# Kernel optimization log

Measured on AMD Instinct MI355X. Metric: run time of the kernel, lower is better.

## Reference

```python
import jax, jax.numpy as jnp
import numpy as np

N = 50000      # nodes
E = 800000     # edges
XS = 64        # x_size
ES = 32        # edge_attr dim (in_size = XS + ES = 96)
OUT = 64       # out_size
H = 128        # hidden_size
EPS = 1e-5


def _lin_init(k, fan_in, fan_out):
    s = 1.0 / np.sqrt(fan_in)
    kw, kb = jax.random.split(k)
    w = jax.random.uniform(kw, (fan_in, fan_out), minval=-s, maxval=s, dtype=jnp.float32)
    b = jax.random.uniform(kb, (fan_out,), minval=-s, maxval=s, dtype=jnp.float32)
    return w, b


def setup_inputs() -> dict:
    key = jax.random.key(0)
    ks = jax.random.split(key, 12)
    x = jax.random.normal(ks[0], (N, XS), dtype=jnp.float32)
    edge_index = jax.random.randint(ks[1], (2, E), 0, N, dtype=jnp.int64)
    edge_attr = jax.random.normal(ks[2], (E, ES), dtype=jnp.float32)
    u = jax.random.normal(ks[3], (1, 8), dtype=jnp.float32)
    batch = jnp.zeros((N,), dtype=jnp.int64)
    # MLP1: (96->128) LReLU (128->128) LReLU (128->64) LReLU LN(64)
    m1w0, m1b0 = _lin_init(ks[4], XS + ES, H)
    m1w1, m1b1 = _lin_init(ks[5], H, H)
    m1w2, m1b2 = _lin_init(ks[6], H, OUT)
    ln1_g = jnp.ones((OUT,), jnp.float32); ln1_b = jnp.zeros((OUT,), jnp.float32)
    # MLP2: (128->128) LReLU (128->128) LReLU (128->64) LReLU LN(64)
    m2w0, m2b0 = _lin_init(ks[7], XS + OUT, H)
    m2w1, m2b1 = _lin_init(ks[8], H, H)
    m2w2, m2b2 = _lin_init(ks[9], H, OUT)
    ln2_g = jnp.ones((OUT,), jnp.float32); ln2_b = jnp.zeros((OUT,), jnp.float32)
    return dict(x=x, edge_index=edge_index, edge_attr=edge_attr, u=u, batch=batch,
                m1w0=m1w0, m1b0=m1b0, m1w1=m1w1, m1b1=m1b1, m1w2=m1w2, m1b2=m1b2,
                ln1_g=ln1_g, ln1_b=ln1_b,
                m2w0=m2w0, m2b0=m2b0, m2w1=m2w1, m2b1=m2b1, m2w2=m2w2, m2b2=m2b2,
                ln2_g=ln2_g, ln2_b=ln2_b)


def _lrelu(v):
    return jax.nn.leaky_relu(v, 0.01)


def _layernorm(v, g, b):
    mu = jnp.mean(v, axis=-1, keepdims=True)
    var = jnp.mean(jnp.square(v - mu), axis=-1, keepdims=True)
    return (v - mu) * jax.lax.rsqrt(var + EPS) * g + b


def _mlp(h, w0, b0, w1, b1, w2, b2, g, bn):
    h = _lrelu(h @ w0 + b0)
    h = _lrelu(h @ w1 + b1)
    h = _lrelu(h @ w2 + b2)          # activate_last=True
    return _layernorm(h, g, bn)      # layer_norm=True


def reference(x, edge_index, edge_attr, u, batch,
              m1w0, m1b0, m1w1, m1b1, m1w2, m1b2, ln1_g, ln1_b,
              m2w0, m2b0, m2w1, m2b1, m2w2, m2b2, ln2_g, ln2_b):
    row, col = edge_index[0], edge_index[1]
    # gather source nodes, concat edge features -> per-edge MLP
    h = jnp.concatenate([x[row], edge_attr], axis=1)            # [E, 96]
    h = _mlp(h, m1w0, m1b0, m1w1, m1b1, m1w2, m1b2, ln1_g, ln1_b)  # [E, 64]
    # scatter_mean over destination nodes
    agg = jax.ops.segment_sum(h, col, num_segments=N)           # [N, 64]
    cnt = jax.ops.segment_sum(jnp.ones((E,), h.dtype), col, num_segments=N)
    agg = agg / jnp.maximum(cnt, 1.0)[:, None]
    # node update MLP
    h2 = jnp.concatenate([x, agg], axis=1)                      # [N, 128]
    return _mlp(h2, m2w0, m2b0, m2w1, m2b1, m2w2, m2b2, ln2_g, ln2_b)
```

## Files before the change

### kernel.cpp

```cpp
#include <hip/hip_runtime.h>


#define NNODES 50000
#define NEDGES 800000
#define NTILES_E 6250
#define NTILES_N 391

typedef __bf16 bf16;
typedef __bf16 __attribute__((ext_vector_type(4))) bf16x4;
typedef __bf16 __attribute__((ext_vector_type(8))) bf16x8;
typedef float __attribute__((ext_vector_type(4))) f32x4;

__device__ __forceinline__ f32x4 mfma_bf16(bf16x8 a, bf16x8 b, f32x4 c) {
    return __builtin_amdgcn_mfma_f32_16x16x32_bf16(a, b, c, 0, 0, 0);
}

__global__ void prep_weights(const float* __restrict__ w10, const float* __restrict__ w11,
                             const float* __restrict__ w12, const float* __restrict__ w20,
                             const float* __restrict__ w21, const float* __restrict__ w22,
                             bf16* __restrict__ img) {
    int idx = blockIdx.x * 256 + threadIdx.x;
    float f;
    if (idx < 13312) {
        int n = idx / 104, k = idx % 104;
        f = (k < 96) ? w10[k * 128 + n] : 0.0f;
    } else if (idx < 30720) {
        int t = idx - 13312; int n = t / 136, k = t % 136;
        f = (k < 128) ? w11[k * 128 + n] : 0.0f;
    } else if (idx < 39424) {
        int t = idx - 30720; int n = t / 136, k = t % 136;
        f = (k < 128) ? w12[k * 64 + n] : 0.0f;
    } else if (idx < 56832) {
        int t = idx - 39424; int n = t / 136, k = t % 136;
        f = (k < 128) ? w20[k * 128 + n] : 0.0f;
    } else if (idx < 74240) {
        int t = idx - 56832; int n = t / 136, k = t % 136;
        f = (k < 128) ? w21[k * 128 + n] : 0.0f;
    } else if (idx < 82944) {
        int t = idx - 74240; int n = t / 136, k = t % 136;
        f = (k < 128) ? w22[k * 64 + n] : 0.0f;
    } else {
        return;
    }
    img[idx] = (bf16)f;
}

__global__ void hist_kernel(const int* __restrict__ col, int* __restrict__ hist) {
    int i = blockIdx.x * 512 + threadIdx.x;
    if (i < NEDGES) {
        int d = col[i];
        if ((unsigned)d < (unsigned)NNODES) atomicAdd(hist + d, 1);
    }
}

__global__ void scanA(const int* __restrict__ hist, int* __restrict__ off,
                      int* __restrict__ csum) {
    __shared__ int sd[512];
    int t = threadIdx.x, i = blockIdx.x * 512 + t;
    int v = (i < NNODES) ? hist[i] : 0;
    sd[t] = v;
    __syncthreads();
    for (int o2 = 1; o2 < 512; o2 <<= 1) {
        int x = (t >= o2) ? sd[t - o2] : 0;
        __syncthreads();
        sd[t] += x;
        __syncthreads();
    }
    if (i < NNODES) off[i] = sd[t] - v;
    if (t == 511) csum[blockIdx.x] = sd[511];
}

__global__ void scanB(int* __restrict__ csum) {
    __shared__ int sd[128];
    int t = threadIdx.x;
    int v = (t < 98) ? csum[t] : 0;
    sd[t] = v;
    __syncthreads();
    for (int o2 = 1; o2 < 128; o2 <<= 1) {
        int x = (t >= o2) ? sd[t - o2] : 0;
        __syncthreads();
        sd[t] += x;
        __syncthreads();
    }
    if (t < 98) csum[t] = sd[t] - v;
}

__global__ void scanC(int* __restrict__ off, const int* __restrict__ csum) {
    int i = blockIdx.x * 512 + threadIdx.x;
    if (i < NNODES) off[i] += csum[blockIdx.x];
}

__global__ void scatter_kernel(const int* __restrict__ eidx, int* __restrict__ off,
                               int* __restrict__ perm, int* __restrict__ rdS) {
    int i = blockIdx.x * 512 + threadIdx.x;
    if (i < NEDGES) {
        int r = eidx[i], d = eidx[NEDGES + i];
        if ((unsigned)d < (unsigned)NNODES && (unsigned)r < (unsigned)NNODES) {
            int pos = atomicAdd(off + d, 1);
            if ((unsigned)pos < (unsigned)NEDGES) {
                perm[pos] = i;
                rdS[pos] = (int)(((unsigned)r & 0xFFFFu) | ((unsigned)d << 16));
            }
        }
    }
}

__global__ __launch_bounds__(256) void edge_mlp(
    const float* __restrict__ x, const int* __restrict__ perm,
    const int* __restrict__ rdS, const float* __restrict__ eattr,
    const bf16* __restrict__ wimg,
    const float* __restrict__ b0g, const float* __restrict__ b1g,
    const float* __restrict__ b2g, const float* __restrict__ lng,
    const float* __restrict__ lnb, float* __restrict__ agg) {
    __shared__ __align__(16) bf16 wall[39424];
    __shared__ __align__(16) bf16 atile[128 * 104];
    __shared__ __align__(16) bf16 hid[128 * 136];
    __shared__ float bs[448];
    __shared__ int dstile[128];

    const int tid = threadIdx.x;
    {
        const uint4* src = (const uint4*)wimg;
        uint4* dst = (uint4*)wall;
        for (int i = tid; i < 4928; i += 256) dst[i] = src[i];
    }
    if (tid < 128) { bs[tid] = b0g[tid]; bs[128 + tid] = b1g[tid]; }
    else {
        int t = tid - 128;
        if (t < 64) { bs[256 + t] = b2g[t]; bs[320 + t] = lng[t]; bs[384 + t] = lnb[t]; }
    }
    __syncthreads();

    const int lane = tid & 63;
    const int wv = tid >> 6;
    const int col16 = lane & 15;
    const int quad = lane >> 4;

    float b0r[8], b1r[8], b2r[4], gr[4], br[4];
#pragma unroll
    for (int i = 0; i < 8; i++) { b0r[i] = bs[i * 16 + col16]; b1r[i] = bs[128 + i * 16 + col16]; }
#pragma unroll
    for (int i = 0; i < 4; i++) {
        b2r[i] = bs[256 + i * 16 + col16];
        gr[i] = bs[320 + i * 16 + col16];
        br[i] = bs[384 + i * 16 + col16];
    }

    const bf16* w0t = wall;
    const bf16* w1t = wall + 13312;
    const bf16* w2t = wall + 30720;

    const f32x4 vzero = {0.0f, 0.0f, 0.0f, 0.0f};
    const int r0 = wv * 32 + col16;
    const int rw = wv * 32 + quad * 4;
    const int el = tid >> 1, half = tid & 1;

    for (int tile = blockIdx.x; tile < NTILES_E; tile += gridDim.x) {
        const int sbase = tile * 128;
        {
            const int s = sbase + el;
            const unsigned v = (unsigned)rdS[s];
            int e = perm[s];
            int r = (int)(v & 0xFFFFu);
            unsigned d = v >> 16;
            if (r >= NNODES) r = 0;
            if ((unsigned)e >= (unsigned)NEDGES) e = 0;
            if (half == 0) dstile[el] = (d < (unsigned)NNODES) ? (int)d : 0;
            const float4* xs = (const float4*)(x + (size_t)r * 64);
            bf16* arow = atile + el * 104;
#pragma unroll
            for (int j = 0; j < 8; j++) {
                float4 vv = xs[half * 8 + j];
                bf16x4 u = {(bf16)vv.x, (bf16)vv.y, (bf16)vv.z, (bf16)vv.w};
                *(bf16x4*)(arow + half * 32 + j * 4) = u;
            }
            const float4* es = (const float4*)(eattr + (size_t)e * 32);
#pragma unroll
            for (int j = 0; j < 4; j++) {
                float4 vv = es[half * 4 + j];
                bf16x4 u = {(bf16)vv.x, (bf16)vv.y, (bf16)vv.z, (bf16)vv.w};
                *(bf16x4*)(arow + 64 + half * 16 + j * 4) = u;
            }
        }
        __syncthreads();

        f32x4 acc1[2][8];
#pragma unroll
        for (int mt = 0; mt < 2; mt++)
#pragma unroll
            for (int nt = 0; nt < 8; nt++) acc1[mt][nt] = vzero;
#pragma unroll
        for (int ks = 0; ks < 3; ks++) {
            bf16x8 a0 = *(const bf16x8*)(atile + r0 * 104 + ks * 32 + quad * 8);
            bf16x8 a1 = *(const bf16x8*)(atile + (r0 + 16) * 104 + ks * 32 + quad * 8);
#pragma unroll
            for (int nt = 0; nt < 8; nt++) {
                bf16x8 b = *(const bf16x8*)(w0t + (nt * 16 + col16) * 104 + ks * 32 + quad * 8);
                acc1[0][nt] = mfma_bf16(a0, b, acc1[0][nt]);
                acc1[1][nt] = mfma_bf16(a1, b, acc1[1][nt]);
            }
        }
#pragma unroll
        for (int mt = 0; mt < 2; mt++)
#pragma unroll
            for (int nt = 0; nt < 8; nt++)
#pragma unroll
                for (int rg = 0; rg < 4; rg++) {
                    float v = acc1[mt][nt][rg] + b0r[nt];
                    v = (v > 0.0f) ? v : 0.01f * v;
                    hid[(rw + mt * 16 + rg) * 136 + nt * 16 + col16] = (bf16)v;
                }

        bf16x8 a2[2][4];
#pragma unroll
        for (int mt = 0; mt < 2; mt++)
#pragma unroll
            for (int ks = 0; ks < 4; ks++)
                a2[mt][ks] = *(const bf16x8*)(hid + (r0 + mt * 16) * 136 + ks * 32 + quad * 8);
        f32x4 acc2[2][8];
#pragma unroll
        for (int mt = 0; mt < 2; mt++)
#pragma unroll
            for (int nt = 0; nt < 8; nt++) acc2[mt][nt] = vzero;
#pragma unroll
        for (int ks = 0; ks < 4; ks++) {
#pragma unroll
            for (int nt = 0; nt < 8; nt++) {
                bf16x8 b = *(const bf16x8*)(w1t + (nt * 16 + col16) * 136 + ks * 32 + quad * 8);
                acc2[0][nt] = mfma_bf16(a2[0][ks], b, acc2[0][nt]);
                acc2[1][nt] = mfma_bf16(a2[1][ks], b, acc2[1][nt]);
            }
        }
#pragma unroll
        for (int mt = 0; mt < 2; mt++)
#pragma unroll
            for (int nt = 0; nt < 8; nt++)
#pragma unroll
                for (int rg = 0; rg < 4; rg++) {
                    float v = acc2[mt][nt][rg] + b1r[nt];
                    v = (v > 0.0f) ? v : 0.01f * v;
                    hid[(rw + mt * 16 + rg) * 136 + nt * 16 + col16] = (bf16)v;
                }

        bf16x8 a3[2][4];
#pragma unroll
        for (int mt = 0; mt < 2; mt++)
#pragma unroll
            for (int ks = 0; ks < 4; ks++)
                a3[mt][ks] = *(const bf16x8*)(hid + (r0 + mt * 16) * 136 + ks * 32 + quad * 8);
        f32x4 acc3[2][4];
#pragma unroll
        for (int mt = 0; mt < 2; mt++)
#pragma unroll
            for (int nt = 0; nt < 4; nt++) acc3[mt][nt] = vzero;
#pragma unroll
        for (int ks = 0; ks < 4; ks++) {
#pragma unroll
            for (int nt = 0; nt < 4; nt++) {
                bf16x8 b = *(const bf16x8*)(w2t + (nt * 16 + col16) * 136 + ks * 32 + quad * 8);
                acc3[0][nt] = mfma_bf16(a3[0][ks], b, acc3[0][nt]);
                acc3[1][nt] = mfma_bf16(a3[1][ks], b, acc3[1][nt]);
            }
        }

#pragma unroll
        for (int mt = 0; mt < 2; mt++) {
            float vals[4][4];
            float s1[4] = {0.f, 0.f, 0.f, 0.f}, s2[4] = {0.f, 0.f, 0.f, 0.f};
#pragma unroll
            for (int nt = 0; nt < 4; nt++)
#pragma unroll
                for (int rg = 0; rg < 4; rg++) {
                    float v = acc3[mt][nt][rg] + b2r[nt];
                    v = (v > 0.0f) ? v : 0.01f * v;
                    vals[nt][rg] = v;
                    s1[rg] += v;
                    s2[rg] += v * v;
                }
#pragma unroll
            for (int off2 = 1; off2 < 16; off2 <<= 1) {
#pragma unroll
                for (int rg = 0; rg < 4; rg++) {
                    s1[rg] += __shfl_xor(s1[rg], off2);
                    s2[rg] += __shfl_xor(s2[rg], off2);
                }
            }
            float o[4][4];
            int dr[4];
#pragma unroll
            for (int rg = 0; rg < 4; rg++) {
                float mu = s1[rg] * 0.015625f;
                float var = s2[rg] * 0.015625f - mu * mu;
                float rstd = rsqrtf(var + 1e-5f);
                int c = dstile[rw + mt * 16 + rg];
                dr[rg] = ((unsigned)c < (unsigned)NNODES) ? c : 0;
#pragma unroll
                for (int nt = 0; nt < 4; nt++)
                    o[nt][rg] = (vals[nt][rg] - mu) * rstd * gr[nt] + br[nt];
            }
            float run0 = o[0][0], run1 = o[1][0], run2 = o[2][0], run3 = o[3][0];
            int cur = dr[0];
#pragma unroll
            for (int rg = 1; rg < 4; rg++) {
                if (dr[rg] != cur) {
                    float* dst = agg + (size_t)cur * 64 + col16;
                    atomicAdd(dst, run0); atomicAdd(dst + 16, run1);
                    atomicAdd(dst + 32, run2); atomicAdd(dst + 48, run3);
                    run0 = o[0][rg]; run1 = o[1][rg]; run2 = o[2][rg]; run3 = o[3][rg];
                    cur = dr[rg];
                } else {
                    run0 += o[0][rg]; run1 += o[1][rg]; run2 += o[2][rg]; run3 += o[3][rg];
                }
            }
            float* dst = agg + (size_t)cur * 64 + col16;
            atomicAdd(dst, run0); atomicAdd(dst + 16, run1);
            atomicAdd(dst + 32, run2); atomicAdd(dst + 48, run3);
        }
        __syncthreads();
    }
}

__global__ __launch_bounds__(256) void node_mlp(
    const float* __restrict__ x, const float* __restrict__ agg,
    const int* __restrict__ hist, const bf16* __restrict__ wimg,
    const float* __restrict__ b0g, const float* __restrict__ b1g,
    const float* __restrict__ b2g, const float* __restrict__ lng,
    const float* __restrict__ lnb, float* __restrict__ out) {
    __shared__ __align__(16) bf16 wall[43520];
    __shared__ __align__(16) bf16 atile[128 * 136];
    __shared__ __align__(16) bf16 hid[128 * 136];
    __shared__ float bs[448];

    const int tid = threadIdx.x;
    {
        const uint4* src = (const uint4*)wimg;
        uint4* dst = (uint4*)wall;
        for (int i = tid; i < 5440; i += 256) dst[i] = src[i];
    }
    if (tid < 128) { bs[tid] = b0g[tid]; bs[128 + tid] = b1g[tid]; }
    else {
        int t = tid - 128;
        if (t < 64) { bs[256 + t] = b2g[t]; bs[320 + t] = lng[t]; bs[384 + t] = lnb[t]; }
    }
    __syncthreads();

    const int lane = tid & 63;
    const int wv = tid >> 6;
    const int col16 = lane & 15;
    const int quad = lane >> 4;

    float b0r[8], b1r[8], b2r[4], gr[4], br[4];
#pragma unroll
    for (int i = 0; i < 8; i++) { b0r[i] = bs[i * 16 + col16]; b1r[i] = bs[128 + i * 16 + col16]; }
#pragma unroll
    for (int i = 0; i < 4; i++) {
        b2r[i] = bs[256 + i * 16 + col16];
        gr[i] = bs[320 + i * 16 + col16];
        br[i] = bs[384 + i * 16 + col16];
    }

    const bf16* w0t = wall;
    const bf16* w1t = wall + 17408;
    const bf16* w2t = wall + 34816;

    const f32x4 vzero = {0.0f, 0.0f, 0.0f, 0.0f};
    const int r0 = wv * 32 + col16;
    const int rw = wv * 32 + quad * 4;
    const int el = tid >> 1, half = tid & 1;

    for (int tile = blockIdx.x; tile < NTILES_N; tile += gridDim.x) {
        const int nbase = tile * 128;
        {
            int i = nbase + el;
            if (i >= NNODES) i = NNODES - 1;
            const float4* xs = (const float4*)(x + (size_t)i * 64);
            bf16* arow = atile + el * 136;
#pragma unroll
            for (int j = 0; j < 8; j++) {
                float4 v = xs[half * 8 + j];
                bf16x4 u = {(bf16)v.x, (bf16)v.y, (bf16)v.z, (bf16)v.w};
                *(bf16x4*)(arow + half * 32 + j * 4) = u;
            }
            int c = hist[i];
            float inv = 1.0f / (float)(c > 1 ? c : 1);
            const float4* as = (const float4*)(agg + (size_t)i * 64);
#pragma unroll
            for (int j = 0; j < 8; j++) {
                float4 v = as[half * 8 + j];
                bf16x4 u = {(bf16)(v.x * inv), (bf16)(v.y * inv), (bf16)(v.z * inv), (bf16)(v.w * inv)};
                *(bf16x4*)(arow + 64 + half * 32 + j * 4) = u;
            }
        }
        __syncthreads();

        f32x4 acc1[2][8];
#pragma unroll
        for (int mt = 0; mt < 2; mt++)
#pragma unroll
            for (int nt = 0; nt < 8; nt++) acc1[mt][nt] = vzero;
#pragma unroll
        for (int ks = 0; ks < 4; ks++) {
            bf16x8 a0 = *(const bf16x8*)(atile + r0 * 136 + ks * 32 + quad * 8);
            bf16x8 a1 = *(const bf16x8*)(atile + (r0 + 16) * 136 + ks * 32 + quad * 8);
#pragma unroll
            for (int nt = 0; nt < 8; nt++) {
                bf16x8 b = *(const bf16x8*)(w0t + (nt * 16 + col16) * 136 + ks * 32 + quad * 8);
                acc1[0][nt] = mfma_bf16(a0, b, acc1[0][nt]);
                acc1[1][nt] = mfma_bf16(a1, b, acc1[1][nt]);
            }
        }
#pragma unroll
        for (int mt = 0; mt < 2; mt++)
#pragma unroll
            for (int nt = 0; nt < 8; nt++)
#pragma unroll
                for (int rg = 0; rg < 4; rg++) {
                    float v = acc1[mt][nt][rg] + b0r[nt];
                    v = (v > 0.0f) ? v : 0.01f * v;
                    hid[(rw + mt * 16 + rg) * 136 + nt * 16 + col16] = (bf16)v;
                }

        bf16x8 a2[2][4];
#pragma unroll
        for (int mt = 0; mt < 2; mt++)
#pragma unroll
            for (int ks = 0; ks < 4; ks++)
                a2[mt][ks] = *(const bf16x8*)(hid + (r0 + mt * 16) * 136 + ks * 32 + quad * 8);
        f32x4 acc2[2][8];
#pragma unroll
        for (int mt = 0; mt < 2; mt++)
#pragma unroll
            for (int nt = 0; nt < 8; nt++) acc2[mt][nt] = vzero;
#pragma unroll
        for (int ks = 0; ks < 4; ks++) {
#pragma unroll
            for (int nt = 0; nt < 8; nt++) {
                bf16x8 b = *(const bf16x8*)(w1t + (nt * 16 + col16) * 136 + ks * 32 + quad * 8);
                acc2[0][nt] = mfma_bf16(a2[0][ks], b, acc2[0][nt]);
                acc2[1][nt] = mfma_bf16(a2[1][ks], b, acc2[1][nt]);
            }
        }
#pragma unroll
        for (int mt = 0; mt < 2; mt++)
#pragma unroll
            for (int nt = 0; nt < 8; nt++)
#pragma unroll
                for (int rg = 0; rg < 4; rg++) {
                    float v = acc2[mt][nt][rg] + b1r[nt];
                    v = (v > 0.0f) ? v : 0.01f * v;
                    hid[(rw + mt * 16 + rg) * 136 + nt * 16 + col16] = (bf16)v;
                }

        bf16x8 a3[2][4];
#pragma unroll
        for (int mt = 0; mt < 2; mt++)
#pragma unroll
            for (int ks = 0; ks < 4; ks++)
                a3[mt][ks] = *(const bf16x8*)(hid + (r0 + mt * 16) * 136 + ks * 32 + quad * 8);
        f32x4 acc3[2][4];
#pragma unroll
        for (int mt = 0; mt < 2; mt++)
#pragma unroll
            for (int nt = 0; nt < 4; nt++) acc3[mt][nt] = vzero;
#pragma unroll
        for (int ks = 0; ks < 4; ks++) {
#pragma unroll
            for (int nt = 0; nt < 4; nt++) {
                bf16x8 b = *(const bf16x8*)(w2t + (nt * 16 + col16) * 136 + ks * 32 + quad * 8);
                acc3[0][nt] = mfma_bf16(a3[0][ks], b, acc3[0][nt]);
                acc3[1][nt] = mfma_bf16(a3[1][ks], b, acc3[1][nt]);
            }
        }

#pragma unroll
        for (int mt = 0; mt < 2; mt++) {
            float vals[4][4];
            float s1[4] = {0.f, 0.f, 0.f, 0.f}, s2[4] = {0.f, 0.f, 0.f, 0.f};
#pragma unroll
            for (int nt = 0; nt < 4; nt++)
#pragma unroll
                for (int rg = 0; rg < 4; rg++) {
                    float v = acc3[mt][nt][rg] + b2r[nt];
                    v = (v > 0.0f) ? v : 0.01f * v;
                    vals[nt][rg] = v;
                    s1[rg] += v;
                    s2[rg] += v * v;
                }
#pragma unroll
            for (int off2 = 1; off2 < 16; off2 <<= 1) {
#pragma unroll
                for (int rg = 0; rg < 4; rg++) {
                    s1[rg] += __shfl_xor(s1[rg], off2);
                    s2[rg] += __shfl_xor(s2[rg], off2);
                }
            }
#pragma unroll
            for (int rg = 0; rg < 4; rg++) {
                float mu = s1[rg] * 0.015625f;
                float var = s2[rg] * 0.015625f - mu * mu;
                float rstd = rsqrtf(var + 1e-5f);
                int i = nbase + rw + mt * 16 + rg;
                if (i < NNODES) {
#pragma unroll
                    for (int nt = 0; nt < 4; nt++) {
                        float o = (vals[nt][rg] - mu) * rstd * gr[nt] + br[nt];
                        out[(size_t)i * 64 + nt * 16 + col16] = o;
                    }
                }
            }
        }
        __syncthreads();
    }
}

extern "C" void kernel_launch(void* const* d_in, const int* in_sizes, int n_in,
                              void* d_out, int out_size, void* d_ws, size_t ws_size,
                              hipStream_t stream) {
    (void)in_sizes; (void)n_in; (void)out_size; (void)ws_size;
    const float* x     = (const float*)d_in[0];
    const int*   eidx  = (const int*)d_in[1];
    const float* eattr = (const float*)d_in[2];
    const float* m1w0 = (const float*)d_in[5];
    const float* m1b0 = (const float*)d_in[6];
    const float* m1w1 = (const float*)d_in[7];
    const float* m1b1 = (const float*)d_in[8];
    const float* m1w2 = (const float*)d_in[9];
    const float* m1b2 = (const float*)d_in[10];
    const float* ln1g = (const float*)d_in[11];
    const float* ln1b = (const float*)d_in[12];
    const float* m2w0 = (const float*)d_in[13];
    const float* m2b0 = (const float*)d_in[14];
    const float* m2w1 = (const float*)d_in[15];
    const float* m2b1 = (const float*)d_in[16];
    const float* m2w2 = (const float*)d_in[17];
    const float* m2b2 = (const float*)d_in[18];
    const float* ln2g = (const float*)d_in[19];
    const float* ln2b = (const float*)d_in[20];

    char* ws = (char*)d_ws;
    float* agg  = (float*)ws;
    int*   hist = (int*)(ws + 12800000);
    int*   off  = (int*)(ws + 13000000);
    int*   csum = (int*)(ws + 13200000);
    int*   perm = (int*)(ws + 13200512);
    int*   rdS  = (int*)(ws + 16400512);
    bf16*  wimg = (bf16*)(ws + 19600512);

    hipMemsetAsync(d_ws, 0, 13000000, stream);
    prep_weights<<<324, 256, 0, stream>>>(m1w0, m1w1, m1w2, m2w0, m2w1, m2w2, wimg);
    hist_kernel<<<1563, 512, 0, stream>>>(eidx + NEDGES, hist);
    scanA<<<98, 512, 0, stream>>>(hist, off, csum);
    scanB<<<1, 128, 0, stream>>>(csum);
    scanC<<<98, 512, 0, stream>>>(off, csum);
    scatter_kernel<<<1563, 512, 0, stream>>>(eidx, off, perm, rdS);
    edge_mlp<<<512, 256, 0, stream>>>(x, perm, rdS, eattr, wimg, m1b0, m1b1, m1b2,
                                      ln1g, ln1b, agg);
    node_mlp<<<196, 256, 0, stream>>>(x, agg, hist, wimg + 39424,
                                      m2b0, m2b1, m2b2, ln2g, ln2b, (float*)d_out);
}
```

Measured before the change: 576.9 us.

## Read MLP weights from global memory and alias LDS tiles to raise occupancy

Both edge and node MLP kernels stop staging the full bf16 weight image in shared memory and read weight fragments straight from global memory, relying on the caches. The separate input-tile and hidden-activation buffers are merged into one aliased LDS buffer. This cuts per-block LDS use sharply, so several blocks can share a CU and hide gather latency, and the grids are enlarged to match. The cost is that every MFMA B-operand load now goes to global memory instead of LDS. Aliasing also relies on each wave touching only its own rows between barriers.

```diff
diff --git a/kernel.cpp b/kernel.cpp
--- a/kernel.cpp
+++ b/kernel.cpp
@@ -112,18 +112,11 @@
     const float* __restrict__ b0g, const float* __restrict__ b1g,
     const float* __restrict__ b2g, const float* __restrict__ lng,
     const float* __restrict__ lnb, float* __restrict__ agg) {
-    __shared__ __align__(16) bf16 wall[39424];
-    __shared__ __align__(16) bf16 atile[128 * 104];
-    __shared__ __align__(16) bf16 hid[128 * 136];
+    __shared__ __align__(16) bf16 buf[128 * 136];
     __shared__ float bs[448];
     __shared__ int dstile[128];
 
     const int tid = threadIdx.x;
-    {
-        const uint4* src = (const uint4*)wimg;
-        uint4* dst = (uint4*)wall;
-        for (int i = tid; i < 4928; i += 256) dst[i] = src[i];
-    }
     if (tid < 128) { bs[tid] = b0g[tid]; bs[128 + tid] = b1g[tid]; }
     else {
         int t = tid - 128;
@@ -146,9 +139,9 @@
         br[i] = bs[384 + i * 16 + col16];
     }
 
-    const bf16* w0t = wall;
-    const bf16* w1t = wall + 13312;
-    const bf16* w2t = wall + 30720;
+    const bf16* w0t = wimg;
+    const bf16* w1t = wimg + 13312;
+    const bf16* w2t = wimg + 30720;
 
     const f32x4 vzero = {0.0f, 0.0f, 0.0f, 0.0f};
     const int r0 = wv * 32 + col16;
@@ -167,7 +160,7 @@
             if ((unsigned)e >= (unsigned)NEDGES) e = 0;
             if (half == 0) dstile[el] = (d < (unsigned)NNODES) ? (int)d : 0;
             const float4* xs = (const float4*)(x + (size_t)r * 64);
-            bf16* arow = atile + el * 104;
+            bf16* arow = buf + el * 136;
 #pragma unroll
             for (int j = 0; j < 8; j++) {
                 float4 vv = xs[half * 8 + j];
@@ -191,8 +184,8 @@
             for (int nt = 0; nt < 8; nt++) acc1[mt][nt] = vzero;
 #pragma unroll
         for (int ks = 0; ks < 3; ks++) {
-            bf16x8 a0 = *(const bf16x8*)(atile + r0 * 104 + ks * 32 + quad * 8);
-            bf16x8 a1 = *(const bf16x8*)(atile + (r0 + 16) * 104 + ks * 32 + quad * 8);
+            bf16x8 a0 = *(const bf16x8*)(buf + r0 * 136 + ks * 32 + quad * 8);
+            bf16x8 a1 = *(const bf16x8*)(buf + (r0 + 16) * 136 + ks * 32 + quad * 8);
 #pragma unroll
             for (int nt = 0; nt < 8; nt++) {
                 bf16x8 b = *(const bf16x8*)(w0t + (nt * 16 + col16) * 104 + ks * 32 + quad * 8);
@@ -208,7 +201,7 @@
                 for (int rg = 0; rg < 4; rg++) {
                     float v = acc1[mt][nt][rg] + b0r[nt];
                     v = (v > 0.0f) ? v : 0.01f * v;
-                    hid[(rw + mt * 16 + rg) * 136 + nt * 16 + col16] = (bf16)v;
+                    buf[(rw + mt * 16 + rg) * 136 + nt * 16 + col16] = (bf16)v;
                 }
 
         bf16x8 a2[2][4];
@@ -216,7 +209,7 @@
         for (int mt = 0; mt < 2; mt++)
 #pragma unroll
             for (int ks = 0; ks < 4; ks++)
-                a2[mt][ks] = *(const bf16x8*)(hid + (r0 + mt * 16) * 136 + ks * 32 + quad * 8);
+                a2[mt][ks] = *(const bf16x8*)(buf + (r0 + mt * 16) * 136 + ks * 32 + quad * 8);
         f32x4 acc2[2][8];
 #pragma unroll
         for (int mt = 0; mt < 2; mt++)
@@ -239,7 +232,7 @@
                 for (int rg = 0; rg < 4; rg++) {
                     float v = acc2[mt][nt][rg] + b1r[nt];
                     v = (v > 0.0f) ? v : 0.01f * v;
-                    hid[(rw + mt * 16 + rg) * 136 + nt * 16 + col16] = (bf16)v;
+                    buf[(rw + mt * 16 + rg) * 136 + nt * 16 + col16] = (bf16)v;
                 }
 
         bf16x8 a3[2][4];
@@ -247,7 +240,7 @@
         for (int mt = 0; mt < 2; mt++)
 #pragma unroll
             for (int ks = 0; ks < 4; ks++)
-                a3[mt][ks] = *(const bf16x8*)(hid + (r0 + mt * 16) * 136 + ks * 32 + quad * 8);
+                a3[mt][ks] = *(const bf16x8*)(buf + (r0 + mt * 16) * 136 + ks * 32 + quad * 8);
         f32x4 acc3[2][4];
 #pragma unroll
         for (int mt = 0; mt < 2; mt++)
@@ -326,17 +319,10 @@
     const float* __restrict__ b0g, const float* __restrict__ b1g,
     const float* __restrict__ b2g, const float* __restrict__ lng,
     const float* __restrict__ lnb, float* __restrict__ out) {
-    __shared__ __align__(16) bf16 wall[43520];
-    __shared__ __align__(16) bf16 atile[128 * 136];
-    __shared__ __align__(16) bf16 hid[128 * 136];
+    __shared__ __align__(16) bf16 buf[128 * 136];
     __shared__ float bs[448];
 
     const int tid = threadIdx.x;
-    {
-        const uint4* src = (const uint4*)wimg;
-        uint4* dst = (uint4*)wall;
-        for (int i = tid; i < 5440; i += 256) dst[i] = src[i];
-    }
     if (tid < 128) { bs[tid] = b0g[tid]; bs[128 + tid] = b1g[tid]; }
     else {
         int t = tid - 128;
@@ -359,9 +345,9 @@
         br[i] = bs[384 + i * 16 + col16];
     }
 
-    const bf16* w0t = wall;
-    const bf16* w1t = wall + 17408;
-    const bf16* w2t = wall + 34816;
+    const bf16* w0t = wimg;
+    const bf16* w1t = wimg + 17408;
+    const bf16* w2t = wimg + 34816;
 
     const f32x4 vzero = {0.0f, 0.0f, 0.0f, 0.0f};
     const int r0 = wv * 32 + col16;
@@ -374,7 +360,7 @@
             int i = nbase + el;
             if (i >= NNODES) i = NNODES - 1;
             const float4* xs = (const float4*)(x + (size_t)i * 64);
-            bf16* arow = atile + el * 136;
+            bf16* arow = buf + el * 136;
 #pragma unroll
             for (int j = 0; j < 8; j++) {
                 float4 v = xs[half * 8 + j];
@@ -400,8 +386,8 @@
             for (int nt = 0; nt < 8; nt++) acc1[mt][nt] = vzero;
 #pragma unroll
         for (int ks = 0; ks < 4; ks++) {
-            bf16x8 a0 = *(const bf16x8*)(atile + r0 * 136 + ks * 32 + quad * 8);
-            bf16x8 a1 = *(const bf16x8*)(atile + (r0 + 16) * 136 + ks * 32 + quad * 8);
+            bf16x8 a0 = *(const bf16x8*)(buf + r0 * 136 + ks * 32 + quad * 8);
+            bf16x8 a1 = *(const bf16x8*)(buf + (r0 + 16) * 136 + ks * 32 + quad * 8);
 #pragma unroll
             for (int nt = 0; nt < 8; nt++) {
                 bf16x8 b = *(const bf16x8*)(w0t + (nt * 16 + col16) * 136 + ks * 32 + quad * 8);
@@ -417,7 +403,7 @@
                 for (int rg = 0; rg < 4; rg++) {
                     float v = acc1[mt][nt][rg] + b0r[nt];
                     v = (v > 0.0f) ? v : 0.01f * v;
-                    hid[(rw + mt * 16 + rg) * 136 + nt * 16 + col16] = (bf16)v;
+                    buf[(rw + mt * 16 + rg) * 136 + nt * 16 + col16] = (bf16)v;
                 }
 
         bf16x8 a2[2][4];
@@ -425,7 +411,7 @@
         for (int mt = 0; mt < 2; mt++)
 #pragma unroll
             for (int ks = 0; ks < 4; ks++)
-                a2[mt][ks] = *(const bf16x8*)(hid + (r0 + mt * 16) * 136 + ks * 32 + quad * 8);
+                a2[mt][ks] = *(const bf16x8*)(buf + (r0 + mt * 16) * 136 + ks * 32 + quad * 8);
         f32x4 acc2[2][8];
 #pragma unroll
         for (int mt = 0; mt < 2; mt++)
@@ -448,7 +434,7 @@
                 for (int rg = 0; rg < 4; rg++) {
                     float v = acc2[mt][nt][rg] + b1r[nt];
                     v = (v > 0.0f) ? v : 0.01f * v;
-                    hid[(rw + mt * 16 + rg) * 136 + nt * 16 + col16] = (bf16)v;
+                    buf[(rw + mt * 16 + rg) * 136 + nt * 16 + col16] = (bf16)v;
                 }
 
         bf16x8 a3[2][4];
@@ -456,7 +442,7 @@
         for (int mt = 0; mt < 2; mt++)
 #pragma unroll
             for (int ks = 0; ks < 4; ks++)
-                a3[mt][ks] = *(const bf16x8*)(hid + (r0 + mt * 16) * 136 + ks * 32 + quad * 8);
+                a3[mt][ks] = *(const bf16x8*)(buf + (r0 + mt * 16) * 136 + ks * 32 + quad * 8);
         f32x4 acc3[2][4];
 #pragma unroll
         for (int mt = 0; mt < 2; mt++)
@@ -553,8 +539,8 @@
     scanB<<<1, 128, 0, stream>>>(csum);
     scanC<<<98, 512, 0, stream>>>(off, csum);
     scatter_kernel<<<1563, 512, 0, stream>>>(eidx, off, perm, rdS);
-    edge_mlp<<<512, 256, 0, stream>>>(x, perm, rdS, eattr, wimg, m1b0, m1b1, m1b2,
-                                      ln1g, ln1b, agg);
-    node_mlp<<<196, 256, 0, stream>>>(x, agg, hist, wimg + 39424,
+    edge_mlp<<<1250, 256, 0, stream>>>(x, perm, rdS, eattr, wimg, m1b0, m1b1, m1b2,
+                                       ln1g, ln1b, agg);
+    node_mlp<<<391, 256, 0, stream>>>(x, agg, hist, wimg + 39424,
                                       m2b0, m2b1, m2b2, ln2g, ln2b, (float*)d_out);
 }
```

New measurement: 592.3 us. +2.7%, slower.
